# Kernel tuning notes

Hardware: AMD Instinct MI355X
Metric: run time of the kernel (lower is better)

Reference implementation:

```python
import jax, jax.numpy as jnp
import numpy as np

U, G, I, D = 10000, 3000, 8000, 32
LAYERS, SOCIAL_LAYERS = 3, 2
NNZ_UI, NNZ_GI = 720000, 440000
L_MEM = 20
B = 4096


def setup_inputs() -> dict:
    key = jax.random.key(0)
    ks = jax.random.split(key, 24)
    s_u = 1.0 / np.sqrt(U).astype(np.float32)
    s_i = 1.0 / np.sqrt(I).astype(np.float32)
    return {
        "group_inputs": jax.random.randint(ks[0], (B,), 0, G, dtype=jnp.int32),
        "item_inputs": jax.random.randint(ks[1], (B,), 0, I, dtype=jnp.int32),
        "user_emb": jax.random.normal(ks[2], (U, D), jnp.float32) * 0.1,
        "group_emb": jax.random.normal(ks[3], (G, D), jnp.float32) * 0.1,
        "item_emb": jax.random.normal(ks[4], (I, D), jnp.float32) * 0.1,
        "ui_rows": jax.random.randint(ks[5], (NNZ_UI,), 0, U + I, dtype=jnp.int32),
        "ui_cols": jax.random.randint(ks[6], (NNZ_UI,), 0, U + I, dtype=jnp.int32),
        "ui_vals": jax.random.uniform(ks[7], (NNZ_UI,), jnp.float32) * 0.02,
        "gi_rows": jax.random.randint(ks[8], (NNZ_GI,), 0, G + I, dtype=jnp.int32),
        "gi_cols": jax.random.randint(ks[9], (NNZ_GI,), 0, G + I, dtype=jnp.int32),
        "gi_vals": jax.random.uniform(ks[10], (NNZ_GI,), jnp.float32) * 0.02,
        "overlap_user": jax.random.normal(ks[11], (U, U), jnp.float32) * (0.1 * s_u),
        "overlap_item": jax.random.normal(ks[12], (I, I), jnp.float32) * (0.1 * s_i),
        "all_group_users": jax.random.randint(ks[13], (G, L_MEM), 0, U, dtype=jnp.int32),
        "all_group_mask": jax.random.uniform(ks[14], (G, L_MEM), jnp.float32) / L_MEM,
        "gate_w1": jax.random.normal(ks[15], (D, D), jnp.float32) * 0.1,
        "gate_b1": jnp.zeros((D,), jnp.float32),
        "gate_w2": jax.random.normal(ks[16], (D, 1), jnp.float32) * 0.1,
        "gate_b2": jnp.zeros((1,), jnp.float32),
        "pred_w1": jax.random.normal(ks[17], (D, 8), jnp.float32) * 0.1,
        "pred_b1": jnp.zeros((8,), jnp.float32),
        "pred_w2": jax.random.normal(ks[18], (8, 1), jnp.float32) * 0.1,
        "pred_b2": jnp.zeros((1,), jnp.float32),
    }


def _spmm(rows, cols, vals, x, n):
    # COO sparse-dense matmul: out[r] += vals * x[c]
    return jax.ops.segment_sum(vals[:, None] * x[cols], rows, num_segments=n)


def reference(group_inputs, item_inputs, user_emb, group_emb, item_emb,
              ui_rows, ui_cols, ui_vals, gi_rows, gi_cols, gi_vals,
              overlap_user, overlap_item, all_group_users, all_group_mask,
              gate_w1, gate_b1, gate_w2, gate_b2,
              pred_w1, pred_b1, pred_w2, pred_b2):
    # ---- GraphConvolution: user-item propagation ----
    ui = jnp.concatenate([user_emb, item_emb])           # [U+I, D]
    embs_ui = [ui]
    for _ in range(LAYERS):
        ui = _spmm(ui_rows, ui_cols, ui_vals, ui, U + I)
        embs_ui.append(ui)
    user_layers = [e[:U] for e in embs_ui]
    item_layers = [e[U:] for e in embs_ui]
    user_emb_for_user = jnp.mean(jnp.stack(user_layers, 1), axis=1)   # [U, D]
    item_emb_for_user = jnp.mean(jnp.stack(item_layers, 1), axis=1)   # [I, D]

    # ---- group-item propagation ----
    gi = jnp.concatenate([group_emb, item_emb_for_user])  # [G+I, D]
    embs_gi = [gi]
    for _ in range(LAYERS):
        gi = _spmm(gi_rows, gi_cols, gi_vals, gi, G + I)
        embs_gi.append(gi)
    group_gi = [e[:G] for e in embs_gi]
    item_gi = [e[G:] for e in embs_gi]
    i_emb = jnp.mean(jnp.stack(item_gi, 1), axis=1)       # [I, D]

    g_layers = []
    for i in range(LAYERS + 1):
        if i % 2 == 0:
            g_layers.append(group_gi[i])
        else:
            emb_in = jnp.concatenate([group_emb, item_layers[i - 1]])
            g_layers.append(_spmm(gi_rows, gi_cols, gi_vals, emb_in, G + I)[:G])
    g_emb = jnp.mean(jnp.stack(g_layers, 1), axis=1)      # [G, D]

    # ---- SocialRelationshipAgg (dense power-series + gathered pooling) ----
    ue = user_emb_for_user
    acc = ue
    for _ in range(SOCIAL_LAYERS):
        ue = overlap_user @ ue
        acc = acc + ue
    members = acc[all_group_users]                        # [G, L, D]
    group_userlayer = jnp.einsum('gl,gld->gd', all_group_mask, members)

    # ---- Gate ----
    x = jnp.concatenate([g_emb, group_userlayer])         # [2G, D]
    h = jax.nn.relu(x @ gate_w1 + gate_b1)
    w = jax.nn.sigmoid(h @ gate_w2 + gate_b2)             # [2G, 1]
    group_final = w[:G] * g_emb + w[G:] * group_userlayer

    # ---- OverlapGraphConvolution on items ----
    it = i_emb
    iacc = it
    for _ in range(SOCIAL_LAYERS):
        it = overlap_item @ it
        iacc = iacc + it

    # ---- Predict ----
    ge = group_final[group_inputs]                        # [B, D]
    ie = iacc[item_inputs]                                # [B, D]
    p = jax.nn.relu((ge * ie) @ pred_w1 + pred_b1)
    return jax.nn.sigmoid(p @ pred_w2 + pred_b2)          # [B, 1]
```

## Files before the change

kernel.cpp:

```cpp
#include <hip/hip_runtime.h>
#include <math.h>

#define U_N 10000
#define G_N 3000
#define I_N 8000
#define D_N 32
#define NNZ_UI 720000
#define NNZ_GI 440000
#define L_MEM 20
#define B_N 4096
#define UI_N (U_N + I_N)
#define GI_N (G_N + I_N)
#define CAP 128
#define KSPLIT 8

static __host__ int cdiv(int a, int b) { return (a + b - 1) / b; }

typedef __attribute__((ext_vector_type(8))) short bf16x8;
typedef __attribute__((ext_vector_type(4))) float f32x4;

__device__ __forceinline__ short f32_to_bf16(float f) {
    unsigned u = __float_as_uint(f);
    unsigned r = (u + 0x7FFFu + ((u >> 16) & 1u)) >> 16;
    return (short)r;
}


__global__ __launch_bounds__(256) void copy_f(float* __restrict__ dst,
                                              const float* __restrict__ src, int n) {
    int i = blockIdx.x * 256 + threadIdx.x;
    if (i < n) dst[i] = src[i];
}

__global__ __launch_bounds__(256) void add_into(float* __restrict__ dst,
                                                const float* __restrict__ src, int n) {
    int i = blockIdx.x * 256 + threadIdx.x;
    if (i < n) dst[i] += src[i];
}

__global__ __launch_bounds__(256) void mean4(const float* __restrict__ a,
                                             const float* __restrict__ b,
                                             const float* __restrict__ c,
                                             const float* __restrict__ d,
                                             float* __restrict__ out, int n) {
    int i = blockIdx.x * 256 + threadIdx.x;
    if (i < n) out[i] = 0.25f * (a[i] + b[i] + c[i] + d[i]);
}


__global__ __launch_bounds__(256) void bucket_fill(const int* __restrict__ rows,
                                                   const int* __restrict__ cols,
                                                   const float* __restrict__ vals,
                                                   int nnz, int* __restrict__ cnt,
                                                   int* __restrict__ bcols,
                                                   float* __restrict__ bvals) {
    int i = blockIdx.x * 256 + threadIdx.x;
    if (i >= nnz) return;
    int r = rows[i];
    int pos = atomicAdd(&cnt[r], 1);
    if (pos < CAP) {
        bcols[(size_t)r * CAP + pos] = cols[i];
        bvals[(size_t)r * CAP + pos] = vals[i];
    }
}

__global__ __launch_bounds__(256) void spmm_bucket(const int* __restrict__ cnt,
                                                   const int* __restrict__ bcols,
                                                   const float* __restrict__ bvals,
                                                   const float* __restrict__ x,
                                                   float* __restrict__ out, int nrows) {
    int row = blockIdx.x * 8 + (threadIdx.x >> 5);
    if (row >= nrows) return;
    int d = threadIdx.x & 31;
    int deg = cnt[row];
    if (deg > CAP) deg = CAP;
    const int* bc = bcols + (size_t)row * CAP;
    const float* bv = bvals + (size_t)row * CAP;
    float acc = 0.f;
    int j = 0;
    for (; j + 1 < deg; j += 2) {
        int c0 = bc[j], c1 = bc[j + 1];
        float v0 = bv[j], v1 = bv[j + 1];
        acc += v0 * x[c0 * 32 + d];
        acc += v1 * x[c1 * 32 + d];
    }
    if (j < deg) acc += bv[j] * x[bc[j] * 32 + d];
    out[(size_t)row * 32 + d] = acc;
}


__global__ __launch_bounds__(256) void pack_xb(const float* __restrict__ x,
                                               short* __restrict__ XB, int N, int ktiles) {
    int idx = blockIdx.x * 256 + threadIdx.x;
    int total = ktiles * 2 * 64;
    if (idx >= total) return;
    int lane = idx & 63;
    int th = idx >> 6;
    int h = th & 1;
    int t = th >> 1;
    int q = lane >> 4;
    int n = (lane & 15) + h * 16;
    short v[8];
#pragma unroll
    for (int j = 0; j < 8; ++j) {
        int c = t * 32 + q * 8 + j;
        v[j] = (c < N) ? f32_to_bf16(x[(size_t)c * 32 + n]) : (short)0;
    }
    short* dst = XB + (size_t)idx * 8;
#pragma unroll
    for (int j = 0; j < 8; ++j) dst[j] = v[j];
}

__global__ __launch_bounds__(256) void dense_mfma(const float* __restrict__ A,
                                                  const short* __restrict__ XB,
                                                  float* __restrict__ out,
                                                  int N, int ktiles) {
    int wid = (blockIdx.x * 256 + threadIdx.x) >> 6;
    int lane = threadIdx.x & 63;
    int strips = N >> 4;
    int strip = wid / KSPLIT;
    int ks = wid - strip * KSPLIT;
    if (strip >= strips) return;
    int r0 = strip << 4;
    int m = lane & 15;
    int q = lane >> 4;
    const float* arow = A + (size_t)(r0 + m) * N + q * 8;
    const bf16x8* xb = (const bf16x8*)XB;
    f32x4 acc0 = {0.f, 0.f, 0.f, 0.f};
    f32x4 acc1 = {0.f, 0.f, 0.f, 0.f};
    for (int t = ks; t < ktiles; t += KSPLIT) {
        int c0 = t * 32;
        bf16x8 afrag;
        if (c0 + 32 <= N) {
            float4 lo = *(const float4*)(arow + c0);
            float4 hi = *(const float4*)(arow + c0 + 4);
            afrag[0] = f32_to_bf16(lo.x); afrag[1] = f32_to_bf16(lo.y);
            afrag[2] = f32_to_bf16(lo.z); afrag[3] = f32_to_bf16(lo.w);
            afrag[4] = f32_to_bf16(hi.x); afrag[5] = f32_to_bf16(hi.y);
            afrag[6] = f32_to_bf16(hi.z); afrag[7] = f32_to_bf16(hi.w);
        } else {
#pragma unroll
            for (int j = 0; j < 8; ++j) {
                int c = c0 + q * 8 + j;
                afrag[j] = (c < N) ? f32_to_bf16(arow[c0 + j]) : (short)0;
            }
        }
        bf16x8 b0 = xb[(size_t)(t * 2 + 0) * 64 + lane];
        bf16x8 b1 = xb[(size_t)(t * 2 + 1) * 64 + lane];
        acc0 = __builtin_amdgcn_mfma_f32_16x16x32_bf16(afrag, b0, acc0, 0, 0, 0);
        acc1 = __builtin_amdgcn_mfma_f32_16x16x32_bf16(afrag, b1, acc1, 0, 0, 0);
    }
#pragma unroll
    for (int i = 0; i < 4; ++i) {
        int row = r0 + q * 4 + i;
        atomicAdd(&out[(size_t)row * 32 + m], acc0[i]);
        atomicAdd(&out[(size_t)row * 32 + m + 16], acc1[i]);
    }
}


__global__ __launch_bounds__(256) void pool_members(const int* __restrict__ users,
                                                    const float* __restrict__ mask,
                                                    const float* __restrict__ accu,
                                                    float* __restrict__ gul) {
    int gid = blockIdx.x * 256 + threadIdx.x;
    if (gid >= G_N * 32) return;
    int g = gid >> 5, d = gid & 31;
    float s = 0.f;
#pragma unroll
    for (int l = 0; l < L_MEM; ++l) {
        int u = users[g * L_MEM + l];
        s += mask[g * L_MEM + l] * accu[(size_t)u * 32 + d];
    }
    gul[gid] = s;
}

__global__ __launch_bounds__(256) void gate_kernel(const float* __restrict__ gemb,
                                                   const float* __restrict__ gul,
                                                   const float* __restrict__ W1,
                                                   const float* __restrict__ b1,
                                                   const float* __restrict__ w2,
                                                   const float* __restrict__ b2,
                                                   float* __restrict__ wout) {
    int row = blockIdx.x * 8 + (threadIdx.x >> 5);
    int j = threadIdx.x & 31;
    if (row >= 2 * G_N) return;
    const float* xrow = (row < G_N) ? (gemb + (size_t)row * 32)
                                    : (gul + (size_t)(row - G_N) * 32);
    float xv = xrow[j];
    float h = b1[j];
#pragma unroll
    for (int k = 0; k < 32; ++k) {
        float xk = __shfl(xv, k, 32);
        h = fmaf(xk, W1[k * 32 + j], h);
    }
    h = fmaxf(h, 0.f);
    float t = h * w2[j];
#pragma unroll
    for (int off = 16; off >= 1; off >>= 1) t += __shfl_xor(t, off, 32);
    if (j == 0) wout[row] = 1.f / (1.f + expf(-(t + b2[0])));
}

__global__ __launch_bounds__(256) void final_mix(const float* __restrict__ wout,
                                                 const float* __restrict__ gemb,
                                                 const float* __restrict__ gul,
                                                 float* __restrict__ gfin) {
    int i = blockIdx.x * 256 + threadIdx.x;
    if (i >= G_N * 32) return;
    int g = i >> 5;
    gfin[i] = wout[g] * gemb[i] + wout[G_N + g] * gul[i];
}

__global__ __launch_bounds__(256) void predict_kernel(const int* __restrict__ gidx,
                                                      const int* __restrict__ iidx,
                                                      const float* __restrict__ gfin,
                                                      const float* __restrict__ iacc,
                                                      const float* __restrict__ pw1,
                                                      const float* __restrict__ pb1,
                                                      const float* __restrict__ pw2,
                                                      const float* __restrict__ pb2,
                                                      float* __restrict__ out) {
    int b = blockIdx.x * 256 + threadIdx.x;
    if (b >= B_N) return;
    const float* ge = gfin + (size_t)gidx[b] * 32;
    const float* ie = iacc + (size_t)iidx[b] * 32;
    float p[8];
#pragma unroll
    for (int j = 0; j < 8; ++j) p[j] = pb1[j];
    for (int d = 0; d < 32; ++d) {
        float t = ge[d] * ie[d];
#pragma unroll
        for (int j = 0; j < 8; ++j) p[j] = fmaf(t, pw1[d * 8 + j], p[j]);
    }
    float s = pb2[0];
#pragma unroll
    for (int j = 0; j < 8; ++j) s = fmaf(fmaxf(p[j], 0.f), pw2[j], s);
    out[b] = 1.f / (1.f + expf(-s));
}


extern "C" void kernel_launch(void* const* d_in, const int* in_sizes, int n_in,
                              void* d_out, int out_size, void* d_ws, size_t ws_size,
                              hipStream_t stream) {
    const int*   gin   = (const int*)d_in[0];
    const int*   iin   = (const int*)d_in[1];
    const float* uemb  = (const float*)d_in[2];
    const float* gemb0 = (const float*)d_in[3];
    const float* iemb0 = (const float*)d_in[4];
    const int*   uir   = (const int*)d_in[5];
    const int*   uic   = (const int*)d_in[6];
    const float* uiv   = (const float*)d_in[7];
    const int*   gir   = (const int*)d_in[8];
    const int*   gic   = (const int*)d_in[9];
    const float* giv   = (const float*)d_in[10];
    const float* ov_u  = (const float*)d_in[11];
    const float* ov_i  = (const float*)d_in[12];
    const int*   agu   = (const int*)d_in[13];
    const float* agm   = (const float*)d_in[14];
    const float* gw1   = (const float*)d_in[15];
    const float* gb1   = (const float*)d_in[16];
    const float* gw2   = (const float*)d_in[17];
    const float* gb2   = (const float*)d_in[18];
    const float* pw1   = (const float*)d_in[19];
    const float* pb1   = (const float*)d_in[20];
    const float* pw2   = (const float*)d_in[21];
    const float* pb2   = (const float*)d_in[22];
    float* out = (float*)d_out;

    const int KT_U = (U_N + 31) / 32;
    const int KT_I = I_N / 32;

    char* wp = (char*)d_ws;
    auto alloc = [&](size_t nbytes) -> void* {
        void* p = (void*)wp;
        wp += (nbytes + 255) & ~(size_t)255;
        return p;
    };
    int*   cnt_ui   = (int*)alloc((size_t)UI_N * 4);
    int*   bcols_ui = (int*)alloc((size_t)UI_N * CAP * 4);
    float* bvals_ui = (float*)alloc((size_t)UI_N * CAP * 4);
    int*   cnt_gi   = (int*)alloc((size_t)GI_N * 4);
    int*   bcols_gi = (int*)alloc((size_t)GI_N * CAP * 4);
    float* bvals_gi = (float*)alloc((size_t)GI_N * CAP * 4);

    float* ui0  = (float*)alloc((size_t)UI_N * 32 * 4);
    float* ui1  = (float*)alloc((size_t)UI_N * 32 * 4);
    float* ui2  = (float*)alloc((size_t)UI_N * 32 * 4);
    float* ui3  = (float*)alloc((size_t)UI_N * 32 * 4);
    float* gi0  = (float*)alloc((size_t)GI_N * 32 * 4);
    float* gi1  = (float*)alloc((size_t)GI_N * 32 * 4);
    float* gi2  = (float*)alloc((size_t)GI_N * 32 * 4);
    float* gi3  = (float*)alloc((size_t)GI_N * 32 * 4);
    float* uefu = (float*)alloc((size_t)U_N * 32 * 4);
    float* iefu = (float*)alloc((size_t)I_N * 32 * 4);
    float* iemb = (float*)alloc((size_t)I_N * 32 * 4);
    float* tmp  = (float*)alloc((size_t)GI_N * 32 * 4);
    float* gt1  = (float*)alloc((size_t)G_N * 32 * 4);
    float* gt3  = (float*)alloc((size_t)G_N * 32 * 4);
    float* gemb = (float*)alloc((size_t)G_N * 32 * 4);
    float* accu = (float*)alloc((size_t)U_N * 32 * 4);
    float* uea  = (float*)alloc((size_t)U_N * 32 * 4);
    float* ueb  = (float*)alloc((size_t)U_N * 32 * 4);
    float* gul  = (float*)alloc((size_t)G_N * 32 * 4);
    float* wg   = (float*)alloc((size_t)2 * G_N * 4);
    float* gfin = (float*)alloc((size_t)G_N * 32 * 4);
    float* iacc = (float*)alloc((size_t)I_N * 32 * 4);
    float* ita  = (float*)alloc((size_t)I_N * 32 * 4);
    float* itb  = (float*)alloc((size_t)I_N * 32 * 4);
    short* xbu  = (short*)alloc((size_t)KT_U * 2 * 64 * 8 * 2);
    short* xbi  = (short*)alloc((size_t)KT_I * 2 * 64 * 8 * 2);

    hipMemsetAsync(cnt_ui, 0, (size_t)UI_N * 4, stream);
    hipMemsetAsync(cnt_gi, 0, (size_t)GI_N * 4, stream);
    bucket_fill<<<cdiv(NNZ_UI, 256), 256, 0, stream>>>(uir, uic, uiv, NNZ_UI,
                                                       cnt_ui, bcols_ui, bvals_ui);
    bucket_fill<<<cdiv(NNZ_GI, 256), 256, 0, stream>>>(gir, gic, giv, NNZ_GI,
                                                       cnt_gi, bcols_gi, bvals_gi);

    copy_f<<<cdiv(U_N * 32, 256), 256, 0, stream>>>(ui0, uemb, U_N * 32);
    copy_f<<<cdiv(I_N * 32, 256), 256, 0, stream>>>(ui0 + (size_t)U_N * 32, iemb0, I_N * 32);
    spmm_bucket<<<cdiv(UI_N, 8), 256, 0, stream>>>(cnt_ui, bcols_ui, bvals_ui, ui0, ui1, UI_N);
    spmm_bucket<<<cdiv(UI_N, 8), 256, 0, stream>>>(cnt_ui, bcols_ui, bvals_ui, ui1, ui2, UI_N);
    spmm_bucket<<<cdiv(UI_N, 8), 256, 0, stream>>>(cnt_ui, bcols_ui, bvals_ui, ui2, ui3, UI_N);
    mean4<<<cdiv(U_N * 32, 256), 256, 0, stream>>>(ui0, ui1, ui2, ui3, uefu, U_N * 32);
    mean4<<<cdiv(I_N * 32, 256), 256, 0, stream>>>(ui0 + (size_t)U_N * 32, ui1 + (size_t)U_N * 32,
                                                   ui2 + (size_t)U_N * 32, ui3 + (size_t)U_N * 32,
                                                   iefu, I_N * 32);

    copy_f<<<cdiv(G_N * 32, 256), 256, 0, stream>>>(gi0, gemb0, G_N * 32);
    copy_f<<<cdiv(I_N * 32, 256), 256, 0, stream>>>(gi0 + (size_t)G_N * 32, iefu, I_N * 32);
    spmm_bucket<<<cdiv(GI_N, 8), 256, 0, stream>>>(cnt_gi, bcols_gi, bvals_gi, gi0, gi1, GI_N);
    spmm_bucket<<<cdiv(GI_N, 8), 256, 0, stream>>>(cnt_gi, bcols_gi, bvals_gi, gi1, gi2, GI_N);
    spmm_bucket<<<cdiv(GI_N, 8), 256, 0, stream>>>(cnt_gi, bcols_gi, bvals_gi, gi2, gi3, GI_N);
    mean4<<<cdiv(I_N * 32, 256), 256, 0, stream>>>(gi0 + (size_t)G_N * 32, gi1 + (size_t)G_N * 32,
                                                   gi2 + (size_t)G_N * 32, gi3 + (size_t)G_N * 32,
                                                   iemb, I_N * 32);

    copy_f<<<cdiv(G_N * 32, 256), 256, 0, stream>>>(tmp, gemb0, G_N * 32);
    copy_f<<<cdiv(I_N * 32, 256), 256, 0, stream>>>(tmp + (size_t)G_N * 32, iemb0, I_N * 32);
    spmm_bucket<<<cdiv(G_N, 8), 256, 0, stream>>>(cnt_gi, bcols_gi, bvals_gi, tmp, gt1, G_N);
    copy_f<<<cdiv(I_N * 32, 256), 256, 0, stream>>>(tmp + (size_t)G_N * 32,
                                                    ui2 + (size_t)U_N * 32, I_N * 32);
    spmm_bucket<<<cdiv(G_N, 8), 256, 0, stream>>>(cnt_gi, bcols_gi, bvals_gi, tmp, gt3, G_N);
    mean4<<<cdiv(G_N * 32, 256), 256, 0, stream>>>(gemb0, gt1, gi2, gt3, gemb, G_N * 32);

    const int U_STRIPS = U_N / 16, I_STRIPS = I_N / 16;
    copy_f<<<cdiv(U_N * 32, 256), 256, 0, stream>>>(accu, uefu, U_N * 32);
    pack_xb<<<cdiv(KT_U * 128, 256), 256, 0, stream>>>(uefu, xbu, U_N, KT_U);
    hipMemsetAsync(uea, 0, (size_t)U_N * 32 * 4, stream);
    dense_mfma<<<cdiv(U_STRIPS * KSPLIT, 4), 256, 0, stream>>>(ov_u, xbu, uea, U_N, KT_U);
    add_into<<<cdiv(U_N * 32, 256), 256, 0, stream>>>(accu, uea, U_N * 32);
    pack_xb<<<cdiv(KT_U * 128, 256), 256, 0, stream>>>(uea, xbu, U_N, KT_U);
    hipMemsetAsync(ueb, 0, (size_t)U_N * 32 * 4, stream);
    dense_mfma<<<cdiv(U_STRIPS * KSPLIT, 4), 256, 0, stream>>>(ov_u, xbu, ueb, U_N, KT_U);
    add_into<<<cdiv(U_N * 32, 256), 256, 0, stream>>>(accu, ueb, U_N * 32);

    pool_members<<<cdiv(G_N * 32, 256), 256, 0, stream>>>(agu, agm, accu, gul);
    gate_kernel<<<cdiv(2 * G_N, 8), 256, 0, stream>>>(gemb, gul, gw1, gb1, gw2, gb2, wg);
    final_mix<<<cdiv(G_N * 32, 256), 256, 0, stream>>>(wg, gemb, gul, gfin);

    copy_f<<<cdiv(I_N * 32, 256), 256, 0, stream>>>(iacc, iemb, I_N * 32);
    pack_xb<<<cdiv(KT_I * 128, 256), 256, 0, stream>>>(iemb, xbi, I_N, KT_I);
    hipMemsetAsync(ita, 0, (size_t)I_N * 32 * 4, stream);
    dense_mfma<<<cdiv(I_STRIPS * KSPLIT, 4), 256, 0, stream>>>(ov_i, xbi, ita, I_N, KT_I);
    add_into<<<cdiv(I_N * 32, 256), 256, 0, stream>>>(iacc, ita, I_N * 32);
    pack_xb<<<cdiv(KT_I * 128, 256), 256, 0, stream>>>(ita, xbi, I_N, KT_I);
    hipMemsetAsync(itb, 0, (size_t)I_N * 32 * 4, stream);
    dense_mfma<<<cdiv(I_STRIPS * KSPLIT, 4), 256, 0, stream>>>(ov_i, xbi, itb, I_N, KT_I);
    add_into<<<cdiv(I_N * 32, 256), 256, 0, stream>>>(iacc, itb, I_N * 32);

    predict_kernel<<<cdiv(B_N, 256), 256, 0, stream>>>(gin, iin, gfin, iacc,
                                                       pw1, pb1, pw2, pb2, out);
}
```

Baseline: 1.175 ms.

## Fuse copies and means, interleave bucket entries, atomically accumulate power series

Removes the copy, add_into and separate mean kernels. The SpMM now reads from two source pointers selected by column index, which replaces the staging copies into concatenated buffers. Bucket columns and values are packed into one int2 array, and the gather loop is unrolled by four. The dense MFMA writes its atomics into both the next-iterate buffer and the running accumulator, and the second power step accumulates straight into the accumulator. Pool, gate and mix are merged into one kernel, and the memsets are combined. The cost is doubled atomics in the first dense pass plus a branchy gather in the SpMM, in exchange for fewer launches and less memory traffic.

```diff
diff --git a/kernel.cpp b/kernel.cpp
--- a/kernel.cpp
+++ b/kernel.cpp
@@ -26,66 +26,93 @@
 }
 
 
-__global__ __launch_bounds__(256) void copy_f(float* __restrict__ dst,
-                                              const float* __restrict__ src, int n) {
-    int i = blockIdx.x * 256 + threadIdx.x;
-    if (i < n) dst[i] = src[i];
-}
-
-__global__ __launch_bounds__(256) void add_into(float* __restrict__ dst,
-                                                const float* __restrict__ src, int n) {
-    int i = blockIdx.x * 256 + threadIdx.x;
-    if (i < n) dst[i] += src[i];
-}
-
-__global__ __launch_bounds__(256) void mean4(const float* __restrict__ a,
-                                             const float* __restrict__ b,
-                                             const float* __restrict__ c,
-                                             const float* __restrict__ d,
-                                             float* __restrict__ out, int n) {
-    int i = blockIdx.x * 256 + threadIdx.x;
-    if (i < n) out[i] = 0.25f * (a[i] + b[i] + c[i] + d[i]);
-}
-
-
 __global__ __launch_bounds__(256) void bucket_fill(const int* __restrict__ rows,
                                                    const int* __restrict__ cols,
                                                    const float* __restrict__ vals,
                                                    int nnz, int* __restrict__ cnt,
-                                                   int* __restrict__ bcols,
-                                                   float* __restrict__ bvals) {
+                                                   int2* __restrict__ bkt) {
     int i = blockIdx.x * 256 + threadIdx.x;
     if (i >= nnz) return;
     int r = rows[i];
     int pos = atomicAdd(&cnt[r], 1);
     if (pos < CAP) {
-        bcols[(size_t)r * CAP + pos] = cols[i];
-        bvals[(size_t)r * CAP + pos] = vals[i];
-    }
-}
-
-__global__ __launch_bounds__(256) void spmm_bucket(const int* __restrict__ cnt,
-                                                   const int* __restrict__ bcols,
-                                                   const float* __restrict__ bvals,
-                                                   const float* __restrict__ x,
-                                                   float* __restrict__ out, int nrows) {
+        int2 e; e.x = cols[i]; e.y = __float_as_int(vals[i]);
+        bkt[(size_t)r * CAP + pos] = e;
+    }
+}
+
+__global__ __launch_bounds__(256) void spmm_split(const int* __restrict__ cnt,
+                                                  const int2* __restrict__ bkt,
+                                                  const float* __restrict__ x1,
+                                                  const float* __restrict__ x2,
+                                                  int split,
+                                                  float* __restrict__ out, int nrows) {
     int row = blockIdx.x * 8 + (threadIdx.x >> 5);
     if (row >= nrows) return;
     int d = threadIdx.x & 31;
     int deg = cnt[row];
     if (deg > CAP) deg = CAP;
-    const int* bc = bcols + (size_t)row * CAP;
-    const float* bv = bvals + (size_t)row * CAP;
+    const int2* bk = bkt + (size_t)row * CAP;
     float acc = 0.f;
     int j = 0;
-    for (; j + 1 < deg; j += 2) {
-        int c0 = bc[j], c1 = bc[j + 1];
-        float v0 = bv[j], v1 = bv[j + 1];
-        acc += v0 * x[c0 * 32 + d];
-        acc += v1 * x[c1 * 32 + d];
-    }
-    if (j < deg) acc += bv[j] * x[bc[j] * 32 + d];
+#define GATHER(e) ((e.x < split) ? x1[(size_t)e.x * 32 + d] \
+                                 : x2[(size_t)(e.x - split) * 32 + d])
+    for (; j + 3 < deg; j += 4) {
+        int2 e0 = bk[j], e1 = bk[j + 1], e2 = bk[j + 2], e3 = bk[j + 3];
+        float g0 = GATHER(e0), g1 = GATHER(e1), g2 = GATHER(e2), g3 = GATHER(e3);
+        acc = fmaf(__int_as_float(e0.y), g0, acc);
+        acc = fmaf(__int_as_float(e1.y), g1, acc);
+        acc = fmaf(__int_as_float(e2.y), g2, acc);
+        acc = fmaf(__int_as_float(e3.y), g3, acc);
+    }
+    for (; j < deg; ++j) {
+        int2 e = bk[j];
+        acc = fmaf(__int_as_float(e.y), GATHER(e), acc);
+    }
+#undef GATHER
     out[(size_t)row * 32 + d] = acc;
+}
+
+
+__global__ __launch_bounds__(256) void mean_ui(const float* __restrict__ uemb,
+                                               const float* __restrict__ iemb0,
+                                               const float* __restrict__ ui1,
+                                               const float* __restrict__ ui2,
+                                               const float* __restrict__ ui3,
+                                               float* __restrict__ uefu,
+                                               float* __restrict__ accu,
+                                               float* __restrict__ iefu) {
+    int idx = blockIdx.x * 256 + threadIdx.x;
+    if (idx >= UI_N * 32) return;
+    const int UOFF = U_N * 32;
+    float base = (idx < UOFF) ? uemb[idx] : iemb0[idx - UOFF];
+    float m = 0.25f * (base + ui1[idx] + ui2[idx] + ui3[idx]);
+    if (idx < UOFF) { uefu[idx] = m; accu[idx] = m; }
+    else iefu[idx - UOFF] = m;
+}
+
+__global__ __launch_bounds__(256) void mean_gi_items(const float* __restrict__ iefu,
+                                                     const float* __restrict__ gi1,
+                                                     const float* __restrict__ gi2,
+                                                     const float* __restrict__ gi3,
+                                                     float* __restrict__ iemb,
+                                                     float* __restrict__ iacc) {
+    int idx = blockIdx.x * 256 + threadIdx.x;
+    if (idx >= I_N * 32) return;
+    const int GOFF = G_N * 32;
+    float m = 0.25f * (iefu[idx] + gi1[GOFF + idx] + gi2[GOFF + idx] + gi3[GOFF + idx]);
+    iemb[idx] = m;
+    iacc[idx] = m;
+}
+
+__global__ __launch_bounds__(256) void mean_g(const float* __restrict__ gemb0,
+                                              const float* __restrict__ gt1,
+                                              const float* __restrict__ gi2,
+                                              const float* __restrict__ gt3,
+                                              float* __restrict__ gemb) {
+    int idx = blockIdx.x * 256 + threadIdx.x;
+    if (idx >= G_N * 32) return;
+    gemb[idx] = 0.25f * (gemb0[idx] + gt1[idx] + gi2[idx] + gt3[idx]);
 }
 
 
@@ -114,6 +141,7 @@
 __global__ __launch_bounds__(256) void dense_mfma(const float* __restrict__ A,
                                                   const short* __restrict__ XB,
                                                   float* __restrict__ out,
+                                                  float* __restrict__ out2,
                                                   int N, int ktiles) {
     int wid = (blockIdx.x * 256 + threadIdx.x) >> 6;
     int lane = threadIdx.x & 63;
@@ -152,63 +180,54 @@
     }
 #pragma unroll
     for (int i = 0; i < 4; ++i) {
-        int row = r0 + q * 4 + i;
-        atomicAdd(&out[(size_t)row * 32 + m], acc0[i]);
-        atomicAdd(&out[(size_t)row * 32 + m + 16], acc1[i]);
-    }
-}
-
-
-__global__ __launch_bounds__(256) void pool_members(const int* __restrict__ users,
-                                                    const float* __restrict__ mask,
-                                                    const float* __restrict__ accu,
-                                                    float* __restrict__ gul) {
-    int gid = blockIdx.x * 256 + threadIdx.x;
-    if (gid >= G_N * 32) return;
-    int g = gid >> 5, d = gid & 31;
-    float s = 0.f;
+        size_t o = (size_t)(r0 + q * 4 + i) * 32 + m;
+        atomicAdd(&out[o], acc0[i]);
+        atomicAdd(&out[o + 16], acc1[i]);
+        if (out2) {
+            atomicAdd(&out2[o], acc0[i]);
+            atomicAdd(&out2[o + 16], acc1[i]);
+        }
+    }
+}
+
+__global__ __launch_bounds__(256) void pool_gate_mix(const int* __restrict__ users,
+                                                     const float* __restrict__ mask,
+                                                     const float* __restrict__ accu,
+                                                     const float* __restrict__ gemb,
+                                                     const float* __restrict__ W1,
+                                                     const float* __restrict__ b1,
+                                                     const float* __restrict__ w2,
+                                                     const float* __restrict__ b2,
+                                                     float* __restrict__ gfin) {
+    int g = blockIdx.x * 8 + (threadIdx.x >> 5);
+    if (g >= G_N) return;
+    int j = threadIdx.x & 31;
+    float gl = 0.f;
 #pragma unroll
     for (int l = 0; l < L_MEM; ++l) {
         int u = users[g * L_MEM + l];
-        s += mask[g * L_MEM + l] * accu[(size_t)u * 32 + d];
-    }
-    gul[gid] = s;
-}
-
-__global__ __launch_bounds__(256) void gate_kernel(const float* __restrict__ gemb,
-                                                   const float* __restrict__ gul,
-                                                   const float* __restrict__ W1,
-                                                   const float* __restrict__ b1,
-                                                   const float* __restrict__ w2,
-                                                   const float* __restrict__ b2,
-                                                   float* __restrict__ wout) {
-    int row = blockIdx.x * 8 + (threadIdx.x >> 5);
-    int j = threadIdx.x & 31;
-    if (row >= 2 * G_N) return;
-    const float* xrow = (row < G_N) ? (gemb + (size_t)row * 32)
-                                    : (gul + (size_t)(row - G_N) * 32);
-    float xv = xrow[j];
-    float h = b1[j];
+        gl = fmaf(mask[g * L_MEM + l], accu[(size_t)u * 32 + j], gl);
+    }
+    float ge = gemb[(size_t)g * 32 + j];
+    float h1 = b1[j], h2 = b1[j];
 #pragma unroll
     for (int k = 0; k < 32; ++k) {
-        float xk = __shfl(xv, k, 32);
-        h = fmaf(xk, W1[k * 32 + j], h);
-    }
-    h = fmaxf(h, 0.f);
-    float t = h * w2[j];
-#pragma unroll
-    for (int off = 16; off >= 1; off >>= 1) t += __shfl_xor(t, off, 32);
-    if (j == 0) wout[row] = 1.f / (1.f + expf(-(t + b2[0])));
-}
-
-__global__ __launch_bounds__(256) void final_mix(const float* __restrict__ wout,
-                                                 const float* __restrict__ gemb,
-                                                 const float* __restrict__ gul,
-                                                 float* __restrict__ gfin) {
-    int i = blockIdx.x * 256 + threadIdx.x;
-    if (i >= G_N * 32) return;
-    int g = i >> 5;
-    gfin[i] = wout[g] * gemb[i] + wout[G_N + g] * gul[i];
+        float w = W1[k * 32 + j];
+        h1 = fmaf(__shfl(ge, k, 32), w, h1);
+        h2 = fmaf(__shfl(gl, k, 32), w, h2);
+    }
+    float w2j = w2[j];
+    float t1 = fmaxf(h1, 0.f) * w2j;
+    float t2 = fmaxf(h2, 0.f) * w2j;
+#pragma unroll
+    for (int off = 16; off >= 1; off >>= 1) {
+        t1 += __shfl_xor(t1, off, 32);
+        t2 += __shfl_xor(t2, off, 32);
+    }
+    float bb = b2[0];
+    float wa = 1.f / (1.f + expf(-(t1 + bb)));
+    float wb = 1.f / (1.f + expf(-(t2 + bb)));
+    gfin[(size_t)g * 32 + j] = wa * ge + wb * gl;
 }
 
 __global__ __launch_bounds__(256) void predict_kernel(const int* __restrict__ gidx,
@@ -276,98 +295,63 @@
         wp += (nbytes + 255) & ~(size_t)255;
         return p;
     };
-    int*   cnt_ui   = (int*)alloc((size_t)UI_N * 4);
-    int*   bcols_ui = (int*)alloc((size_t)UI_N * CAP * 4);
-    float* bvals_ui = (float*)alloc((size_t)UI_N * CAP * 4);
-    int*   cnt_gi   = (int*)alloc((size_t)GI_N * 4);
-    int*   bcols_gi = (int*)alloc((size_t)GI_N * CAP * 4);
-    float* bvals_gi = (float*)alloc((size_t)GI_N * CAP * 4);
-
-    float* ui0  = (float*)alloc((size_t)UI_N * 32 * 4);
+    int*   cnt_ui = (int*)alloc((size_t)UI_N * 4);
+    int*   cnt_gi = (int*)alloc((size_t)GI_N * 4);
+    int2*  bkt_ui = (int2*)alloc((size_t)UI_N * CAP * 8);
+    int2*  bkt_gi = (int2*)alloc((size_t)GI_N * CAP * 8);
+    float* uea  = (float*)alloc((size_t)U_N * 32 * 4);
+    float* ita  = (float*)alloc((size_t)I_N * 32 * 4);
+
     float* ui1  = (float*)alloc((size_t)UI_N * 32 * 4);
     float* ui2  = (float*)alloc((size_t)UI_N * 32 * 4);
     float* ui3  = (float*)alloc((size_t)UI_N * 32 * 4);
-    float* gi0  = (float*)alloc((size_t)GI_N * 32 * 4);
     float* gi1  = (float*)alloc((size_t)GI_N * 32 * 4);
     float* gi2  = (float*)alloc((size_t)GI_N * 32 * 4);
     float* gi3  = (float*)alloc((size_t)GI_N * 32 * 4);
     float* uefu = (float*)alloc((size_t)U_N * 32 * 4);
     float* iefu = (float*)alloc((size_t)I_N * 32 * 4);
     float* iemb = (float*)alloc((size_t)I_N * 32 * 4);
-    float* tmp  = (float*)alloc((size_t)GI_N * 32 * 4);
     float* gt1  = (float*)alloc((size_t)G_N * 32 * 4);
     float* gt3  = (float*)alloc((size_t)G_N * 32 * 4);
     float* gemb = (float*)alloc((size_t)G_N * 32 * 4);
     float* accu = (float*)alloc((size_t)U_N * 32 * 4);
-    float* uea  = (float*)alloc((size_t)U_N * 32 * 4);
-    float* ueb  = (float*)alloc((size_t)U_N * 32 * 4);
-    float* gul  = (float*)alloc((size_t)G_N * 32 * 4);
-    float* wg   = (float*)alloc((size_t)2 * G_N * 4);
     float* gfin = (float*)alloc((size_t)G_N * 32 * 4);
     float* iacc = (float*)alloc((size_t)I_N * 32 * 4);
-    float* ita  = (float*)alloc((size_t)I_N * 32 * 4);
-    float* itb  = (float*)alloc((size_t)I_N * 32 * 4);
     short* xbu  = (short*)alloc((size_t)KT_U * 2 * 64 * 8 * 2);
     short* xbi  = (short*)alloc((size_t)KT_I * 2 * 64 * 8 * 2);
 
-    hipMemsetAsync(cnt_ui, 0, (size_t)UI_N * 4, stream);
-    hipMemsetAsync(cnt_gi, 0, (size_t)GI_N * 4, stream);
-    bucket_fill<<<cdiv(NNZ_UI, 256), 256, 0, stream>>>(uir, uic, uiv, NNZ_UI,
-                                                       cnt_ui, bcols_ui, bvals_ui);
-    bucket_fill<<<cdiv(NNZ_GI, 256), 256, 0, stream>>>(gir, gic, giv, NNZ_GI,
-                                                       cnt_gi, bcols_gi, bvals_gi);
-
-    copy_f<<<cdiv(U_N * 32, 256), 256, 0, stream>>>(ui0, uemb, U_N * 32);
-    copy_f<<<cdiv(I_N * 32, 256), 256, 0, stream>>>(ui0 + (size_t)U_N * 32, iemb0, I_N * 32);
-    spmm_bucket<<<cdiv(UI_N, 8), 256, 0, stream>>>(cnt_ui, bcols_ui, bvals_ui, ui0, ui1, UI_N);
-    spmm_bucket<<<cdiv(UI_N, 8), 256, 0, stream>>>(cnt_ui, bcols_ui, bvals_ui, ui1, ui2, UI_N);
-    spmm_bucket<<<cdiv(UI_N, 8), 256, 0, stream>>>(cnt_ui, bcols_ui, bvals_ui, ui2, ui3, UI_N);
-    mean4<<<cdiv(U_N * 32, 256), 256, 0, stream>>>(ui0, ui1, ui2, ui3, uefu, U_N * 32);
-    mean4<<<cdiv(I_N * 32, 256), 256, 0, stream>>>(ui0 + (size_t)U_N * 32, ui1 + (size_t)U_N * 32,
-                                                   ui2 + (size_t)U_N * 32, ui3 + (size_t)U_N * 32,
-                                                   iefu, I_N * 32);
-
-    copy_f<<<cdiv(G_N * 32, 256), 256, 0, stream>>>(gi0, gemb0, G_N * 32);
-    copy_f<<<cdiv(I_N * 32, 256), 256, 0, stream>>>(gi0 + (size_t)G_N * 32, iefu, I_N * 32);
-    spmm_bucket<<<cdiv(GI_N, 8), 256, 0, stream>>>(cnt_gi, bcols_gi, bvals_gi, gi0, gi1, GI_N);
-    spmm_bucket<<<cdiv(GI_N, 8), 256, 0, stream>>>(cnt_gi, bcols_gi, bvals_gi, gi1, gi2, GI_N);
-    spmm_bucket<<<cdiv(GI_N, 8), 256, 0, stream>>>(cnt_gi, bcols_gi, bvals_gi, gi2, gi3, GI_N);
-    mean4<<<cdiv(I_N * 32, 256), 256, 0, stream>>>(gi0 + (size_t)G_N * 32, gi1 + (size_t)G_N * 32,
-                                                   gi2 + (size_t)G_N * 32, gi3 + (size_t)G_N * 32,
-                                                   iemb, I_N * 32);
-
-    copy_f<<<cdiv(G_N * 32, 256), 256, 0, stream>>>(tmp, gemb0, G_N * 32);
-    copy_f<<<cdiv(I_N * 32, 256), 256, 0, stream>>>(tmp + (size_t)G_N * 32, iemb0, I_N * 32);
-    spmm_bucket<<<cdiv(G_N, 8), 256, 0, stream>>>(cnt_gi, bcols_gi, bvals_gi, tmp, gt1, G_N);
-    copy_f<<<cdiv(I_N * 32, 256), 256, 0, stream>>>(tmp + (size_t)G_N * 32,
-                                                    ui2 + (size_t)U_N * 32, I_N * 32);
-    spmm_bucket<<<cdiv(G_N, 8), 256, 0, stream>>>(cnt_gi, bcols_gi, bvals_gi, tmp, gt3, G_N);
-    mean4<<<cdiv(G_N * 32, 256), 256, 0, stream>>>(gemb0, gt1, gi2, gt3, gemb, G_N * 32);
+    hipMemsetAsync(cnt_ui, 0, (size_t)(UI_N + GI_N) * 4 + 256, stream);
+    bucket_fill<<<cdiv(NNZ_UI, 256), 256, 0, stream>>>(uir, uic, uiv, NNZ_UI, cnt_ui, bkt_ui);
+    bucket_fill<<<cdiv(NNZ_GI, 256), 256, 0, stream>>>(gir, gic, giv, NNZ_GI, cnt_gi, bkt_gi);
+    hipMemsetAsync(uea, 0, (size_t)(U_N + I_N) * 32 * 4 + 256, stream);
+
+    spmm_split<<<cdiv(UI_N, 8), 256, 0, stream>>>(cnt_ui, bkt_ui, uemb, iemb0, U_N, ui1, UI_N);
+    spmm_split<<<cdiv(UI_N, 8), 256, 0, stream>>>(cnt_ui, bkt_ui, ui1, ui1 + (size_t)U_N * 32, U_N, ui2, UI_N);
+    spmm_split<<<cdiv(UI_N, 8), 256, 0, stream>>>(cnt_ui, bkt_ui, ui2, ui2 + (size_t)U_N * 32, U_N, ui3, UI_N);
+    mean_ui<<<cdiv(UI_N * 32, 256), 256, 0, stream>>>(uemb, iemb0, ui1, ui2, ui3, uefu, accu, iefu);
+
+    spmm_split<<<cdiv(GI_N, 8), 256, 0, stream>>>(cnt_gi, bkt_gi, gemb0, iefu, G_N, gi1, GI_N);
+    spmm_split<<<cdiv(GI_N, 8), 256, 0, stream>>>(cnt_gi, bkt_gi, gi1, gi1 + (size_t)G_N * 32, G_N, gi2, GI_N);
+    spmm_split<<<cdiv(GI_N, 8), 256, 0, stream>>>(cnt_gi, bkt_gi, gi2, gi2 + (size_t)G_N * 32, G_N, gi3, GI_N);
+    mean_gi_items<<<cdiv(I_N * 32, 256), 256, 0, stream>>>(iefu, gi1, gi2, gi3, iemb, iacc);
+
+    spmm_split<<<cdiv(G_N, 8), 256, 0, stream>>>(cnt_gi, bkt_gi, gemb0, iemb0, G_N, gt1, G_N);
+    spmm_split<<<cdiv(G_N, 8), 256, 0, stream>>>(cnt_gi, bkt_gi, gemb0, ui2 + (size_t)U_N * 32, G_N, gt3, G_N);
+    mean_g<<<cdiv(G_N * 32, 256), 256, 0, stream>>>(gemb0, gt1, gi2, gt3, gemb);
 
     const int U_STRIPS = U_N / 16, I_STRIPS = I_N / 16;
-    copy_f<<<cdiv(U_N * 32, 256), 256, 0, stream>>>(accu, uefu, U_N * 32);
     pack_xb<<<cdiv(KT_U * 128, 256), 256, 0, stream>>>(uefu, xbu, U_N, KT_U);
-    hipMemsetAsync(uea, 0, (size_t)U_N * 32 * 4, stream);
-    dense_mfma<<<cdiv(U_STRIPS * KSPLIT, 4), 256, 0, stream>>>(ov_u, xbu, uea, U_N, KT_U);
-    add_into<<<cdiv(U_N * 32, 256), 256, 0, stream>>>(accu, uea, U_N * 32);
+    dense_mfma<<<cdiv(U_STRIPS * KSPLIT, 4), 256, 0, stream>>>(ov_u, xbu, uea, accu, U_N, KT_U);
     pack_xb<<<cdiv(KT_U * 128, 256), 256, 0, stream>>>(uea, xbu, U_N, KT_U);
-    hipMemsetAsync(ueb, 0, (size_t)U_N * 32 * 4, stream);
-    dense_mfma<<<cdiv(U_STRIPS * KSPLIT, 4), 256, 0, stream>>>(ov_u, xbu, ueb, U_N, KT_U);
-    add_into<<<cdiv(U_N * 32, 256), 256, 0, stream>>>(accu, ueb, U_N * 32);
-
-    pool_members<<<cdiv(G_N * 32, 256), 256, 0, stream>>>(agu, agm, accu, gul);
-    gate_kernel<<<cdiv(2 * G_N, 8), 256, 0, stream>>>(gemb, gul, gw1, gb1, gw2, gb2, wg);
-    final_mix<<<cdiv(G_N * 32, 256), 256, 0, stream>>>(wg, gemb, gul, gfin);
-
-    copy_f<<<cdiv(I_N * 32, 256), 256, 0, stream>>>(iacc, iemb, I_N * 32);
+    dense_mfma<<<cdiv(U_STRIPS * KSPLIT, 4), 256, 0, stream>>>(ov_u, xbu, accu, nullptr, U_N, KT_U);
+
+    pool_gate_mix<<<cdiv(G_N, 8), 256, 0, stream>>>(agu, agm, accu, gemb,
+                                                    gw1, gb1, gw2, gb2, gfin);
+
     pack_xb<<<cdiv(KT_I * 128, 256), 256, 0, stream>>>(iemb, xbi, I_N, KT_I);
-    hipMemsetAsync(ita, 0, (size_t)I_N * 32 * 4, stream);
-    dense_mfma<<<cdiv(I_STRIPS * KSPLIT, 4), 256, 0, stream>>>(ov_i, xbi, ita, I_N, KT_I);
-    add_into<<<cdiv(I_N * 32, 256), 256, 0, stream>>>(iacc, ita, I_N * 32);
+    dense_mfma<<<cdiv(I_STRIPS * KSPLIT, 4), 256, 0, stream>>>(ov_i, xbi, ita, iacc, I_N, KT_I);
     pack_xb<<<cdiv(KT_I * 128, 256), 256, 0, stream>>>(ita, xbi, I_N, KT_I);
-    hipMemsetAsync(itb, 0, (size_t)I_N * 32 * 4, stream);
-    dense_mfma<<<cdiv(I_STRIPS * KSPLIT, 4), 256, 0, stream>>>(ov_i, xbi, itb, I_N, KT_I);
-    add_into<<<cdiv(I_N * 32, 256), 256, 0, stream>>>(iacc, itb, I_N * 32);
+    dense_mfma<<<cdiv(I_STRIPS * KSPLIT, 4), 256, 0, stream>>>(ov_i, xbi, iacc, nullptr, I_N, KT_I);
 
     predict_kernel<<<cdiv(B_N, 256), 256, 0, stream>>>(gin, iin, gfin, iacc,
                                                        pw1, pb1, pw2, pb2, out);
```

Result: faster. 1.087 ms (-7.5%).
